# Performance work log

Hardware: AMD Instinct MI355X
Metric: run time of the kernel (lower is better)

The kernel has to match this reference:

```python
import jax, jax.numpy as jnp
import numpy as np

B, FC, FR, L, H, E, GH = 2048, 171, 171, 32, 256, 16, 64
IN = L + FC      # 203: decoder input_size
INT = L + H      # 288: decoder inter_size
OUT = FR         # 171: output_size (num_future_predictions=1)


def _forward(x, c, eps, fc1_w, fc1_b, fc2_w, fc2_b, mu_w, mu_b, lv_w, lv_b,
             g0_w, g0_b, g1_w, g1_b, g2_w, g2_b, w0, b0, w1, b1, w2, b2):
    elu = jax.nn.elu
    # Encoder_up
    h1 = elu(jnp.concatenate([x, c], axis=1) @ fc1_w + fc1_b)
    h2 = elu(jnp.concatenate([x, h1], axis=1) @ fc2_w + fc2_b)
    s = jnp.concatenate([x, h2], axis=1)
    mu = s @ mu_w + mu_b
    logvar = s @ lv_w + lv_b
    # reparameterize (eps supplied externally for determinism)
    z = mu + eps * jnp.exp(0.5 * logvar)
    # MixedDecoder_up gate -> softmax coefficients [B, E]
    g = elu(jnp.concatenate([z, c], axis=1) @ g0_w + g0_b)
    g = elu(g @ g1_w + g1_b)
    coef = jax.nn.softmax(g @ g2_w + g2_b, axis=1)
    # soft-MoE blended layers: mixed_weight = coef @ expert weights, then per-sample matvec
    layer = c
    for W, bb, act in ((w0, b0, True), (w1, b1, True), (w2, b2, False)):
        inp = jnp.concatenate([z, layer], axis=1)           # [B, in]
        mixed_w = jnp.einsum('be,eio->bio', coef, W)        # [B, in, out] (matches torch matmul+view)
        out = jnp.einsum('bi,bio->bo', inp, mixed_w) + coef @ bb  # baddbmm
        layer = jax.nn.elu(out) if act else out
    return layer, mu, logvar


def setup_inputs() -> dict:
    key = jax.random.key(0)
    ks = jax.random.split(key, 20)
    r = jax.random.normal

    def w(k, i, o):
        return (r(k, (i, o), jnp.float32) / np.sqrt(i)).astype(jnp.float32)

    return {
        'x': r(ks[0], (B, FR), jnp.float32),
        'c': r(ks[1], (B, FC), jnp.float32),
        'eps': r(ks[2], (B, L), jnp.float32),
        # Encoder_up params (stored as [in, out])
        'fc1_w': w(ks[3], FC + FR, H), 'fc1_b': jnp.zeros((H,), jnp.float32),
        'fc2_w': w(ks[4], FR + H, H), 'fc2_b': jnp.zeros((H,), jnp.float32),
        'mu_w': w(ks[5], FR + H, L), 'mu_b': jnp.zeros((L,), jnp.float32),
        'lv_w': w(ks[6], FR + H, L), 'lv_b': jnp.zeros((L,), jnp.float32),
        # gate MLP
        'g0_w': w(ks[7], IN, GH), 'g0_b': jnp.zeros((GH,), jnp.float32),
        'g1_w': w(ks[8], GH, GH), 'g1_b': jnp.zeros((GH,), jnp.float32),
        'g2_w': w(ks[9], GH, E), 'g2_b': jnp.zeros((E,), jnp.float32),
        # expert weights [E, in, out], biases filled with 0.01 as in the source
        'w0': (r(ks[10], (E, IN, H), jnp.float32) / np.sqrt(IN)).astype(jnp.float32),
        'b0': jnp.full((E, H), 0.01, jnp.float32),
        'w1': (r(ks[11], (E, INT, H), jnp.float32) / np.sqrt(INT)).astype(jnp.float32),
        'b1': jnp.full((E, H), 0.01, jnp.float32),
        'w2': (r(ks[12], (E, INT, OUT), jnp.float32) / np.sqrt(INT)).astype(jnp.float32),
        'b2': jnp.full((E, OUT), 0.01, jnp.float32),
    }


def reference(x, c, eps, fc1_w, fc1_b, fc2_w, fc2_b, mu_w, mu_b, lv_w, lv_b,
              g0_w, g0_b, g1_w, g1_b, g2_w, g2_b, w0, b0, w1, b1, w2, b2):
    return _forward(x, c, eps, fc1_w, fc1_b, fc2_w, fc2_b, mu_w, mu_b, lv_w, lv_b,
                    g0_w, g0_b, g1_w, g1_b, g2_w, g2_b, w0, b0, w1, b1, w2, b2)
```

## Files before the change

kernel.cpp:

```cpp
#include <hip/hip_runtime.h>
#include <math.h>

#define NB   2048
#define NFC  171
#define NFR  171
#define NL   32
#define NH   256
#define NE   16
#define NGH  64
#define NIN  203
#define NINT 288
#define NOUT 171

typedef __attribute__((ext_vector_type(8))) short bf16x8;
typedef __attribute__((ext_vector_type(4))) float f32x4;

__device__ __forceinline__ float elu_f(float v) {
    return v > 0.0f ? v : expm1f(v);
}

__device__ __forceinline__ short f2bf(float f) {
    unsigned u = __float_as_uint(f);
    unsigned r = (u + 0x7FFFu + ((u >> 16) & 1u)) >> 16;
    return (short)r;
}

__device__ __forceinline__ void gload16(void* lds, const void* g) {
    __builtin_amdgcn_global_load_lds(
        (const __attribute__((address_space(1))) unsigned*)g,
        (__attribute__((address_space(3))) unsigned*)lds, 16, 0, 0);
}

template<int N> __device__ __forceinline__ void waitcnt_vm() {
    if constexpr (N == 0)      asm volatile("s_waitcnt vmcnt(0) lgkmcnt(0)" ::: "memory");
    else if constexpr (N == 1) asm volatile("s_waitcnt vmcnt(1) lgkmcnt(0)" ::: "memory");
    else if constexpr (N == 2) asm volatile("s_waitcnt vmcnt(2) lgkmcnt(0)" ::: "memory");
    else                       asm volatile("s_waitcnt vmcnt(4) lgkmcnt(0)" ::: "memory");
}
__device__ __forceinline__ void loop_sync(int s, int NS) {
    if (s + 3 < NS)      waitcnt_vm<2>();
    else if (s + 2 < NS) waitcnt_vm<1>();
    else                 waitcnt_vm<0>();
    __builtin_amdgcn_s_barrier();
}
__device__ __forceinline__ void loop_sync64(int s, int NS) {
    if (s + 3 < NS)      waitcnt_vm<4>();
    else if (s + 2 < NS) waitcnt_vm<2>();
    else                 waitcnt_vm<0>();
    __builtin_amdgcn_s_barrier();
}

__global__ __launch_bounds__(256) void prep_all(
    const float* s0, const float* s1, const float* s2, const float* s3,
    const float* s4, const float* s5, const float* s6,
    const float* s7, const float* s8, const float* s9,
    short* d0, short* d1, short* d2, short* d3,
    short* d4, short* d5, short* d6, short* d7, short* d8, short* d9,
    const float* __restrict__ x, const float* __restrict__ c,
    short* __restrict__ xc, short* __restrict__ xh1, short* __restrict__ xh2,
    short* __restrict__ inp0)
{
    __shared__ float T[32][33];
    const int tid = threadIdx.x;

    if (blockIdx.x >= 3168) {
        const int b = blockIdx.x - 3168;
        for (int i = tid; i < 384; i += 256) {
            float v = (i < 171) ? x[b * 171 + i] : ((i < 342) ? c[b * 171 + (i - 171)] : 0.0f);
            xc[(size_t)b * 384 + i] = f2bf(v);
        }
        for (int i = tid; i < 171; i += 256) {
            short v = f2bf(x[b * 171 + i]);
            xh1[(size_t)b * 448 + i] = v;
            xh2[(size_t)b * 448 + i] = v;
        }
        for (int i = tid; i < 21; i += 256) {
            xh1[(size_t)b * 448 + 427 + i] = 0;
            xh2[(size_t)b * 448 + 427 + i] = 0;
        }
        for (int i = tid; i < 192; i += 256) {
            inp0[(size_t)b * 224 + 32 + i] = (i < 171) ? f2bf(c[b * 171 + i]) : (short)0;
        }
        return;
    }

    constexpr int K_[10]   = {342, 427, 427, 427, 203, 288, 288, 203,  64,  64};
    constexpr int O_[10]   = {256, 256,  32,  32, 256, 256, 171,  64,  64,  16};
    constexpr int KP_[10]  = {384, 448, 448, 448, 224, 288, 288, 224,  64,  64};
    constexpr int OP_[10]  = {256, 256,  64,  64, 256, 256, 192,  64,  64,  32};
    constexpr int nKT_[10] = { 12,  14,  14,  14,   7,   9,   9,   7,   2,   2};
    constexpr int tpe_[10] = { 96, 112,  14,  14,  56,  72,  54,  14,   4,   2};
    constexpr int st_[10]  = {  0,  96, 208, 222, 236,1132,2284,3148,3162,3166};
    const float* srcs[10] = {s0, s1, s2, s3, s4, s5, s6, s7, s8, s9};
    short*       dsts[10] = {d0, d1, d2, d3, d4, d5, d6, d7, d8, d9};

    int t = blockIdx.x;
    int s = 0;
    while (s < 9 && t >= st_[s + 1]) ++s;
    int local = t - st_[s];
    int e = local / tpe_[s];
    int rem = local - e * tpe_[s];
    int ox = rem / nKT_[s];
    int ky = rem - ox * nKT_[s];
    const int K = K_[s], O = O_[s], KP = KP_[s], OP = OP_[s];
    const float* src = srcs[s];
    short* dst = dsts[s];

    const int cc = tid & 31, r0 = tid >> 5;
#pragma unroll
    for (int i = 0; i < 4; ++i) {
        int r = r0 + i * 8;
        int gk = ky * 32 + r, go = ox * 32 + cc;
        T[r][cc] = (gk < K && go < O) ? src[((size_t)e * K + gk) * O + go] : 0.0f;
    }
    __syncthreads();
#pragma unroll
    for (int i = 0; i < 4; ++i) {
        int r = r0 + i * 8;
        int go = ox * 32 + r, gk = ky * 32 + cc;
        dst[((size_t)e * OP + go) * KP + gk] = f2bf(T[cc][r]);
    }
}

template<int KP>
__global__ __launch_bounds__(256, 2) void enc_gemm(
    const short* __restrict__ A,
    const short* __restrict__ Wt,
    const float* __restrict__ bias,
    short* __restrict__ dst, int dstld, int dstoff)
{
    constexpr int NKS = KP / 64;
    constexpr int CHR = KP / 8;

    __shared__ short As[32 * KP];
    __shared__ short Bs[4][64 * 64];

    const int tid = threadIdx.x;
    const int lane = tid & 63;
    const int wid = tid >> 6;
    const int wm = wid & 1, wn = wid >> 1;
    const int brow = blockIdx.y * 32, bcol = blockIdx.x * 64;
    const int wbase = wid * 1024;
    const int kseg = lane >> 4;

#pragma unroll
    for (int i = 0; i < (32 * CHR) / 256; ++i) {
        int ch = i * 256 + tid;
        int r = ch / CHR, kc = ch - r * CHR;
        int kcs = kc ^ ((r >> 1) & 3);
        gload16((char*)As + i * 4096 + wbase, A + (size_t)(brow + r) * KP + kcs * 8);
    }
    auto stageB = [&](int buf, int ks) {
#pragma unroll
        for (int g = 0; g < 2; ++g) {
            int ch = g * 256 + tid;
            int o = ch >> 3, sl = ch & 7;
            int sp = sl ^ ((o >> 1) & 3);
            gload16((char*)Bs[buf] + g * 4096 + wbase,
                    Wt + (size_t)(bcol + o) * KP + ks * 64 + sp * 8);
        }
    };
    stageB(0, 0); stageB(1, 1); stageB(2, 2);
    waitcnt_vm<4>();
    __builtin_amdgcn_s_barrier();

    const f32x4 zero4 = {0.0f, 0.0f, 0.0f, 0.0f};
    f32x4 acc[2] = {zero4, zero4};

    for (int s = 0; s < NKS; ++s) {
        if (s + 3 < NKS) stageB((s + 3) & 3, s + 3);
#pragma unroll
        for (int kk = 0; kk < 2; ++kk) {
            bf16x8 a, b[2];
            int rr = wm * 16 + (lane & 15);
            int kcp = (s * 8 + kk * 4 + kseg) ^ ((rr >> 1) & 3);
            a = *(const bf16x8*)&As[rr * KP + kcp * 8];
#pragma unroll
            for (int nr = 0; nr < 2; ++nr) {
                int oo = wn * 32 + nr * 16 + (lane & 15);
                int sp = (kk * 4 + kseg) ^ ((oo >> 1) & 3);
                b[nr] = *(const bf16x8*)&Bs[s & 3][oo * 64 + sp * 8];
            }
#pragma unroll
            for (int nr = 0; nr < 2; ++nr)
                acc[nr] = __builtin_amdgcn_mfma_f32_16x16x32_bf16(a, b[nr], acc[nr], 0, 0, 0);
        }
        loop_sync64(s, NKS);
    }

#pragma unroll
    for (int j = 0; j < 4; ++j) {
        int row = brow + wm * 16 + kseg * 4 + j;
#pragma unroll
        for (int nr = 0; nr < 2; ++nr) {
            int col = bcol + wn * 32 + nr * 16 + (lane & 15);
            float v = acc[nr][j] + bias[col];
            dst[(size_t)row * dstld + dstoff + col] = f2bf(elu_f(v));
        }
    }
}

__global__ __launch_bounds__(256) void mulvz_gate(
    const short* __restrict__ A,
    const short* __restrict__ Wt,
    const float* __restrict__ mub, const float* __restrict__ lvb,
    const float* __restrict__ eps,
    const short* __restrict__ g0wt,
    const short* __restrict__ g1wt,
    const short* __restrict__ g2wt,
    const float* __restrict__ g0b, const float* __restrict__ g1b,
    const float* __restrict__ g2b,
    float* __restrict__ mu_out, float* __restrict__ lv_out,
    short* __restrict__ inp0, short* __restrict__ inp1, short* __restrict__ inp2,
    float* __restrict__ coef)
{
    constexpr int KP = 448;
    constexpr int NKS = KP / 64;
    constexpr int CHR = KP / 8;

    __shared__ short As[32 * 448];
    __shared__ short Bs[4][64 * 64];
    __shared__ float Els[32][32];
    __shared__ short gA[32 * 224];
    __shared__ short g0s[64 * 224];
    __shared__ short g1s[64 * 64];
    __shared__ short g2s[32 * 64];
    __shared__ short hA[32 * 64];
    __shared__ short hB[32 * 64];

    const int tid = threadIdx.x;
    const int lane = tid & 63;
    const int wid = tid >> 6;
    const int wm = wid & 1, wn = wid >> 1;
    const int brow = blockIdx.y * 32;
    const int wbase = wid * 1024;
    const int kseg = lane >> 4;
    const int l15 = lane & 15;

#pragma unroll
    for (int i = 0; i < 7; ++i) {
        int ch = i * 256 + tid;
        int r = ch / CHR, kc = ch - r * CHR;
        int kcs = kc ^ ((r >> 1) & 3);
        gload16((char*)As + i * 4096 + wbase, A + (size_t)(brow + r) * KP + kcs * 8);
    }
#pragma unroll
    for (int i = 0; i < 4; ++i) {
        int ch = i * 256 + tid;
        if (ch < 896) {
            int r = ch / 28, kc = ch - r * 28;
            int kcs = kc ^ ((r >> 1) & 3);
            gload16((char*)gA + i * 4096 + wbase, inp0 + (size_t)(brow + r) * 224 + kcs * 8);
        }
    }
#pragma unroll
    for (int i = 0; i < 7; ++i) {
        int ch = i * 256 + tid;
        int r = ch / 28, kc = ch - r * 28;
        int kcs = kc ^ ((r >> 1) & 3);
        gload16((char*)g0s + i * 4096 + wbase, g0wt + (size_t)r * 224 + kcs * 8);
    }
#pragma unroll
    for (int i = 0; i < 2; ++i) {
        int ch = i * 256 + tid;
        int r = ch >> 3, kc = ch & 7;
        int kcs = kc ^ ((r >> 1) & 3);
        gload16((char*)g1s + i * 4096 + wbase, g1wt + (size_t)r * 64 + kcs * 8);
    }
    {
        int ch = tid;
        int r = ch >> 3, kc = ch & 7;
        int kcs = kc ^ ((r >> 1) & 3);
        gload16((char*)g2s + wbase, g2wt + (size_t)r * 64 + kcs * 8);
    }
    auto stageB = [&](int buf, int ks) {
#pragma unroll
        for (int g = 0; g < 2; ++g) {
            int ch = g * 256 + tid;
            int o = ch >> 3, sl = ch & 7;
            int sp = sl ^ ((o >> 1) & 3);
            gload16((char*)Bs[buf] + g * 4096 + wbase,
                    Wt + (size_t)o * KP + ks * 64 + sp * 8);
        }
    };
    stageB(0, 0); stageB(1, 1); stageB(2, 2);
    waitcnt_vm<4>();
    __builtin_amdgcn_s_barrier();

    const f32x4 zero4 = {0.0f, 0.0f, 0.0f, 0.0f};
    f32x4 acc[2] = {zero4, zero4};

    for (int s = 0; s < NKS; ++s) {
        if (s + 3 < NKS) stageB((s + 3) & 3, s + 3);
#pragma unroll
        for (int kk = 0; kk < 2; ++kk) {
            bf16x8 av, b[2];
            int rr = wm * 16 + l15;
            int kcp = (s * 8 + kk * 4 + kseg) ^ ((rr >> 1) & 3);
            av = *(const bf16x8*)&As[rr * KP + kcp * 8];
#pragma unroll
            for (int nr = 0; nr < 2; ++nr) {
                int oo = wn * 32 + nr * 16 + l15;
                int sp = (kk * 4 + kseg) ^ ((oo >> 1) & 3);
                b[nr] = *(const bf16x8*)&Bs[s & 3][oo * 64 + sp * 8];
            }
#pragma unroll
            for (int nr = 0; nr < 2; ++nr)
                acc[nr] = __builtin_amdgcn_mfma_f32_16x16x32_bf16(av, b[nr], acc[nr], 0, 0, 0);
        }
        loop_sync64(s, NKS);
    }

#pragma unroll
    for (int j = 0; j < 4; ++j) {
        int rl = wm * 16 + kseg * 4 + j;
        int row = brow + rl;
#pragma unroll
        for (int nr = 0; nr < 2; ++nr) {
            int cc = nr * 16 + l15;
            if (wn == 1) {
                float v = acc[nr][j] + lvb[cc];
                lv_out[(size_t)row * 32 + cc] = v;
                Els[rl][cc] = expf(0.5f * v);
            } else {
                float v = acc[nr][j] + mub[cc];
                mu_out[(size_t)row * 32 + cc] = v;
                acc[nr][j] = v;
            }
        }
    }
    __syncthreads();
    if (wn == 0) {
#pragma unroll
        for (int j = 0; j < 4; ++j) {
            int rl = wm * 16 + kseg * 4 + j;
            int row = brow + rl;
#pragma unroll
            for (int nr = 0; nr < 2; ++nr) {
                int cc = nr * 16 + l15;
                float z = acc[nr][j] + eps[(size_t)row * 32 + cc] * Els[rl][cc];
                short zb = f2bf(z);
                inp0[(size_t)row * 224 + cc] = zb;
                inp1[(size_t)row * 288 + cc] = zb;
                inp2[(size_t)row * 288 + cc] = zb;
                int swz = (cc >> 3) ^ ((rl >> 1) & 3);
                gA[rl * 224 + swz * 8 + (cc & 7)] = zb;
            }
        }
    }
    __syncthreads();

    {
        f32x4 g[2] = {zero4, zero4};
#pragma unroll
        for (int s = 0; s < 7; ++s) {
            bf16x8 av, b[2];
            int rr = wm * 16 + l15;
            int kcp = (s * 4 + kseg) ^ ((rr >> 1) & 3);
            av = *(const bf16x8*)&gA[rr * 224 + kcp * 8];
#pragma unroll
            for (int nr = 0; nr < 2; ++nr) {
                int oo = wn * 32 + nr * 16 + l15;
                int sp = (s * 4 + kseg) ^ ((oo >> 1) & 3);
                b[nr] = *(const bf16x8*)&g0s[oo * 224 + sp * 8];
            }
#pragma unroll
            for (int nr = 0; nr < 2; ++nr)
                g[nr] = __builtin_amdgcn_mfma_f32_16x16x32_bf16(av, b[nr], g[nr], 0, 0, 0);
        }
#pragma unroll
        for (int j = 0; j < 4; ++j) {
            int rl = wm * 16 + kseg * 4 + j;
#pragma unroll
            for (int nr = 0; nr < 2; ++nr) {
                int cc = wn * 32 + nr * 16 + l15;
                float v = elu_f(g[nr][j] + g0b[cc]);
                int swz = (cc >> 3) ^ ((rl >> 1) & 3);
                hA[rl * 64 + swz * 8 + (cc & 7)] = f2bf(v);
            }
        }
    }
    __syncthreads();
    {
        f32x4 g[2] = {zero4, zero4};
#pragma unroll
        for (int s = 0; s < 2; ++s) {
            bf16x8 av, b[2];
            int rr = wm * 16 + l15;
            int kcp = (s * 4 + kseg) ^ ((rr >> 1) & 3);
            av = *(const bf16x8*)&hA[rr * 64 + kcp * 8];
#pragma unroll
            for (int nr = 0; nr < 2; ++nr) {
                int oo = wn * 32 + nr * 16 + l15;
                int sp = (s * 4 + kseg) ^ ((oo >> 1) & 3);
                b[nr] = *(const bf16x8*)&g1s[oo * 64 + sp * 8];
            }
#pragma unroll
            for (int nr = 0; nr < 2; ++nr)
                g[nr] = __builtin_amdgcn_mfma_f32_16x16x32_bf16(av, b[nr], g[nr], 0, 0, 0);
        }
#pragma unroll
        for (int j = 0; j < 4; ++j) {
            int rl = wm * 16 + kseg * 4 + j;
#pragma unroll
            for (int nr = 0; nr < 2; ++nr) {
                int cc = wn * 32 + nr * 16 + l15;
                float v = elu_f(g[nr][j] + g1b[cc]);
                int swz = (cc >> 3) ^ ((rl >> 1) & 3);
                hB[rl * 64 + swz * 8 + (cc & 7)] = f2bf(v);
            }
        }
    }
    __syncthreads();
    if (wn == 0) {
        f32x4 g = zero4;
#pragma unroll
        for (int s = 0; s < 2; ++s) {
            bf16x8 av, b;
            int rr = wm * 16 + l15;
            int kcp = (s * 4 + kseg) ^ ((rr >> 1) & 3);
            av = *(const bf16x8*)&hB[rr * 64 + kcp * 8];
            int oo = l15;
            int sp = (s * 4 + kseg) ^ ((oo >> 1) & 3);
            b = *(const bf16x8*)&g2s[oo * 64 + sp * 8];
            g = __builtin_amdgcn_mfma_f32_16x16x32_bf16(av, b, g, 0, 0, 0);
        }
        float bv = g2b[l15];
#pragma unroll
        for (int j = 0; j < 4; ++j) {
            int rl = wm * 16 + kseg * 4 + j;
            int row = brow + rl;
            float a2 = g[j] + bv;
            float m = a2;
            for (int off = 1; off < 16; off <<= 1) m = fmaxf(m, __shfl_xor(m, off, 16));
            float ev = expf(a2 - m);
            float sm = ev;
            for (int off = 1; off < 16; off <<= 1) sm += __shfl_xor(sm, off, 16);
            coef[(size_t)row * 16 + l15] = ev / sm;
        }
    }
}

template<int KP, int OP, int EPG>
__global__ __launch_bounds__(256, 2) void moe_gemm(
    const short* __restrict__ inp,
    const short* __restrict__ Wt,
    const float* __restrict__ coef,
    float* __restrict__ partial)
{
    constexpr int NKS = KP / 32;
    constexpr int CHR = KP / 8;
    constexpr int NS = EPG * NKS;

    __shared__ short As[64 * KP];
    __shared__ short Bs[4][64 * 32];
    __shared__ float Cs[64][16];

    const int tid = threadIdx.x;
    const int lane = tid & 63;
    const int wid = tid >> 6;
    const int wm = wid >> 1, wn = wid & 1;
    const int bn = blockIdx.x, bm = blockIdx.y, kg = blockIdx.z;
    const int brow = bm * 64, bcol = bn * 64;
    const int wbase = wid * 1024;
    const int kseg = lane >> 4;

    {
        int r = tid >> 2, q = tid & 3;
        float4 v = ((const float4*)(coef + (size_t)(brow + r) * 16))[q];
        *(float4*)&Cs[r][q * 4] = v;
    }
#pragma unroll
    for (int i = 0; i < (64 * KP / 8) / 256; ++i) {
        int ch = i * 256 + tid;
        int r = ch / CHR, kc = ch - r * CHR;
        int kcs = kc ^ ((r >> 1) & 3);
        gload16((char*)As + i * 4096 + wbase,
                inp + (size_t)(brow + r) * KP + kcs * 8);
    }
    auto stageB = [&](int buf, int s) {
        int ei = s / NKS, ks = s - ei * NKS;
        int e = kg * EPG + ei;
        int o = tid >> 2, sl = tid & 3;
        int sp = sl ^ ((o >> 1) & 3);
        gload16((char*)Bs[buf] + wbase,
                Wt + (size_t)(e * OP + bcol + o) * KP + ks * 32 + sp * 8);
    };
    stageB(0, 0); stageB(1, 1); stageB(2, 2);
    waitcnt_vm<2>();
    __builtin_amdgcn_s_barrier();

    const f32x4 zero4 = {0.0f, 0.0f, 0.0f, 0.0f};
    f32x4 outacc[2][2] = {{zero4, zero4}, {zero4, zero4}};
    f32x4 acc[2][2];

    for (int s = 0; s < NS; ++s) {
        int ei = s / NKS, ks = s - ei * NKS;
        if (ks == 0) {
            acc[0][0] = zero4; acc[0][1] = zero4;
            acc[1][0] = zero4; acc[1][1] = zero4;
        }
        if (s + 3 < NS) stageB((s + 3) & 3, s + 3);

        bf16x8 a[2], b[2];
#pragma unroll
        for (int mr = 0; mr < 2; ++mr) {
            int rr = wm * 32 + mr * 16 + (lane & 15);
            int kcr = ks * 4 + kseg;
            int kcp = kcr ^ ((rr >> 1) & 3);
            a[mr] = *(const bf16x8*)&As[rr * KP + kcp * 8];
        }
#pragma unroll
        for (int nr = 0; nr < 2; ++nr) {
            int oo = wn * 32 + nr * 16 + (lane & 15);
            int sp = kseg ^ ((oo >> 1) & 3);
            b[nr] = *(const bf16x8*)&Bs[s & 3][oo * 32 + sp * 8];
        }
#pragma unroll
        for (int mr = 0; mr < 2; ++mr)
#pragma unroll
            for (int nr = 0; nr < 2; ++nr)
                acc[mr][nr] = __builtin_amdgcn_mfma_f32_16x16x32_bf16(
                    a[mr], b[nr], acc[mr][nr], 0, 0, 0);

        if (ks == NKS - 1) {
            int e = kg * EPG + ei;
#pragma unroll
            for (int mr = 0; mr < 2; ++mr) {
                int rb = wm * 32 + mr * 16 + kseg * 4;
#pragma unroll
                for (int j = 0; j < 4; ++j) {
                    float cfv = Cs[rb + j][e];
#pragma unroll
                    for (int nr = 0; nr < 2; ++nr)
                        outacc[mr][nr][j] += cfv * acc[mr][nr][j];
                }
            }
        }
        loop_sync(s, NS);
    }

    float* pout = partial + (size_t)kg * 2048 * OP;
#pragma unroll
    for (int mr = 0; mr < 2; ++mr)
#pragma unroll
        for (int j = 0; j < 4; ++j) {
            int row = brow + wm * 32 + mr * 16 + kseg * 4 + j;
#pragma unroll
            for (int nr = 0; nr < 2; ++nr) {
                int col = bcol + wn * 32 + nr * 16 + (lane & 15);
                pout[(size_t)row * OP + col] = outacc[mr][nr][j];
            }
        }
}

template<int NP, int O, bool ACT, int NKG>
__global__ __launch_bounds__(256) void moe_finish(
    const float* __restrict__ partial,
    const float* __restrict__ coef,
    const float* __restrict__ bb,
    short* __restrict__ nxt,
    float* __restrict__ fout)
{
    __shared__ float bbs[16 * O];
    __shared__ float cfs[8][16];
    const int tid = threadIdx.x;
    const int row0 = blockIdx.x * 8;

    for (int i = tid; i < 16 * O; i += 256) bbs[i] = bb[i];
    if (tid < 128) cfs[tid >> 4][tid & 15] = coef[(row0 + (tid >> 4)) * 16 + (tid & 15)];
    __syncthreads();

    constexpr int NG = NP / 4;
    for (int idx = tid; idx < 8 * NG; idx += 256) {
        int r = idx / NG, og = idx - r * NG;
        int o = og * 4;
        int row = row0 + r;
        float4 v = {0.f, 0.f, 0.f, 0.f};
#pragma unroll
        for (int kg = 0; kg < NKG; ++kg) {
            float4 p = *(const float4*)&partial[(size_t)(kg * 2048 + row) * NP + o];
            v.x += p.x; v.y += p.y; v.z += p.z; v.w += p.w;
        }
        float vv[4] = {v.x, v.y, v.z, v.w};
#pragma unroll
        for (int t = 0; t < 4; ++t) {
            int oo = o + t;
            if (oo < O) {
                float bias = 0.0f;
#pragma unroll
                for (int e = 0; e < 16; ++e) bias += cfs[r][e] * bbs[e * O + oo];
                float val = vv[t] + bias;
                if (ACT) val = elu_f(val);
                if (nxt) nxt[(size_t)row * 288 + 32 + oo] = f2bf(val);
                else     fout[(size_t)row * O + oo] = val;
            }
        }
    }
}

extern "C" void kernel_launch(void* const* d_in, const int* in_sizes, int n_in,
                              void* d_out, int out_size, void* d_ws, size_t ws_size,
                              hipStream_t stream)
{
    const float* x    = (const float*)d_in[0];
    const float* c    = (const float*)d_in[1];
    const float* eps  = (const float*)d_in[2];
    const float* fc1w = (const float*)d_in[3];
    const float* fc1b = (const float*)d_in[4];
    const float* fc2w = (const float*)d_in[5];
    const float* fc2b = (const float*)d_in[6];
    const float* muw  = (const float*)d_in[7];
    const float* mub  = (const float*)d_in[8];
    const float* lvw  = (const float*)d_in[9];
    const float* lvb  = (const float*)d_in[10];
    const float* g0w  = (const float*)d_in[11];
    const float* g0b  = (const float*)d_in[12];
    const float* g1w  = (const float*)d_in[13];
    const float* g1b  = (const float*)d_in[14];
    const float* g2w  = (const float*)d_in[15];
    const float* g2b  = (const float*)d_in[16];
    const float* w0   = (const float*)d_in[17];
    const float* b0   = (const float*)d_in[18];
    const float* w1   = (const float*)d_in[19];
    const float* b1   = (const float*)d_in[20];
    const float* w2   = (const float*)d_in[21];
    const float* b2   = (const float*)d_in[22];

    float* out       = (float*)d_out;
    float* out_layer = out;
    float* out_mu    = out + NB * NOUT;
    float* out_lv    = out_mu + NB * NL;

    float* ws      = (float*)d_ws;
    float* partial = ws;
    float* cf      = partial + 8 * 2048 * 256;
    short* xc    = (short*)(cf + 32768);
    short* xh1   = xc   + (size_t)2048 * 384;
    short* xh2   = xh1  + (size_t)2048 * 448;
    short* inp0  = xh2  + (size_t)2048 * 448;
    short* inp1  = inp0 + (size_t)2048 * 224;
    short* inp2  = inp1 + (size_t)2048 * 288;
    short* fc1Wt = inp2 + (size_t)2048 * 288;
    short* fc2Wt = fc1Wt + 256 * 384;
    short* mlWt  = fc2Wt + 256 * 448;
    short* Wt0   = mlWt + 64 * 448;
    short* Wt1   = Wt0 + 16 * 256 * 224;
    short* Wt2   = Wt1 + 16 * 256 * 288;
    short* g0wt  = Wt2 + 16 * 192 * 288;
    short* g1wt  = g0wt + 64 * 224;
    short* g2wt  = g1wt + 64 * 64;

    dim3 blk(256);

    prep_all<<<dim3(3168 + 2048), blk, 0, stream>>>(
        fc1w, fc2w, muw, lvw, w0, w1, w2, g0w, g1w, g2w,
        fc1Wt, fc2Wt, mlWt, mlWt + 32 * 448, Wt0, Wt1, Wt2, g0wt, g1wt, g2wt,
        x, c, xc, xh1, xh2, inp0);

    enc_gemm<384><<<dim3(4, 64), blk, 0, stream>>>(xc,  fc1Wt, fc1b, xh1, 448, 171);
    enc_gemm<448><<<dim3(4, 64), blk, 0, stream>>>(xh1, fc2Wt, fc2b, xh2, 448, 171);
    mulvz_gate<<<dim3(1, 64), blk, 0, stream>>>(
        xh2, mlWt, mub, lvb, eps, g0wt, g1wt, g2wt, g0b, g1b, g2b,
        out_mu, out_lv, inp0, inp1, inp2, cf);

    moe_gemm<224, 256, 4><<<dim3(4, 32, 4), blk, 0, stream>>>(inp0, Wt0, cf, partial);
    moe_finish<256, 256, true, 4><<<dim3(256), blk, 0, stream>>>(partial, cf, b0, inp1, nullptr);
    moe_gemm<288, 256, 4><<<dim3(4, 32, 4), blk, 0, stream>>>(inp1, Wt1, cf, partial);
    moe_finish<256, 256, true, 4><<<dim3(256), blk, 0, stream>>>(partial, cf, b1, inp2, nullptr);
    moe_gemm<288, 192, 4><<<dim3(3, 32, 4), blk, 0, stream>>>(inp2, Wt2, cf, partial);
    moe_finish<192, 171, false, 4><<<dim3(256), blk, 0, stream>>>(partial, cf, b2, nullptr, out_layer);
}
```

Baseline: 120.3 us.

## Deepen MoE GEMM prefetch pipeline and split experts into more k-groups

```diff
diff --git a/kernel.cpp b/kernel.cpp
--- a/kernel.cpp
+++ b/kernel.cpp
@@ -35,18 +35,21 @@
     if constexpr (N == 0)      asm volatile("s_waitcnt vmcnt(0) lgkmcnt(0)" ::: "memory");
     else if constexpr (N == 1) asm volatile("s_waitcnt vmcnt(1) lgkmcnt(0)" ::: "memory");
     else if constexpr (N == 2) asm volatile("s_waitcnt vmcnt(2) lgkmcnt(0)" ::: "memory");
+    else if constexpr (N == 3) asm volatile("s_waitcnt vmcnt(3) lgkmcnt(0)" ::: "memory");
     else                       asm volatile("s_waitcnt vmcnt(4) lgkmcnt(0)" ::: "memory");
-}
-__device__ __forceinline__ void loop_sync(int s, int NS) {
-    if (s + 3 < NS)      waitcnt_vm<2>();
-    else if (s + 2 < NS) waitcnt_vm<1>();
-    else                 waitcnt_vm<0>();
-    __builtin_amdgcn_s_barrier();
 }
 __device__ __forceinline__ void loop_sync64(int s, int NS) {
     if (s + 3 < NS)      waitcnt_vm<4>();
     else if (s + 2 < NS) waitcnt_vm<2>();
     else                 waitcnt_vm<0>();
+    __builtin_amdgcn_s_barrier();
+}
+__device__ __forceinline__ void phase_sync(int rem) {
+    if (rem >= 6)      waitcnt_vm<4>();
+    else if (rem == 5) waitcnt_vm<3>();
+    else if (rem == 4) waitcnt_vm<2>();
+    else if (rem == 3) waitcnt_vm<1>();
+    else               waitcnt_vm<0>();
     __builtin_amdgcn_s_barrier();
 }
 
@@ -453,7 +456,7 @@
     constexpr int NS = EPG * NKS;
 
     __shared__ short As[64 * KP];
-    __shared__ short Bs[4][64 * 32];
+    __shared__ short Bs[8][64 * 32];
     __shared__ float Cs[64][16];
 
     const int tid = threadIdx.x;
@@ -464,6 +467,7 @@
     const int brow = bm * 64, bcol = bn * 64;
     const int wbase = wid * 1024;
     const int kseg = lane >> 4;
+    const int l15 = lane & 15;
 
     {
         int r = tid >> 2, q = tid & 3;
@@ -487,34 +491,32 @@
                 Wt + (size_t)(e * OP + bcol + o) * KP + ks * 32 + sp * 8);
     };
     stageB(0, 0); stageB(1, 1); stageB(2, 2);
-    waitcnt_vm<2>();
+    stageB(3, 3); stageB(4, 4); stageB(5, 5);
+    waitcnt_vm<4>();
     __builtin_amdgcn_s_barrier();
 
     const f32x4 zero4 = {0.0f, 0.0f, 0.0f, 0.0f};
     f32x4 outacc[2][2] = {{zero4, zero4}, {zero4, zero4}};
     f32x4 acc[2][2];
 
-    for (int s = 0; s < NS; ++s) {
+    auto do_step = [&](int s) {
         int ei = s / NKS, ks = s - ei * NKS;
         if (ks == 0) {
             acc[0][0] = zero4; acc[0][1] = zero4;
             acc[1][0] = zero4; acc[1][1] = zero4;
         }
-        if (s + 3 < NS) stageB((s + 3) & 3, s + 3);
-
         bf16x8 a[2], b[2];
 #pragma unroll
         for (int mr = 0; mr < 2; ++mr) {
-            int rr = wm * 32 + mr * 16 + (lane & 15);
-            int kcr = ks * 4 + kseg;
-            int kcp = kcr ^ ((rr >> 1) & 3);
+            int rr = wm * 32 + mr * 16 + l15;
+            int kcp = (ks * 4 + kseg) ^ ((rr >> 1) & 3);
             a[mr] = *(const bf16x8*)&As[rr * KP + kcp * 8];
         }
 #pragma unroll
         for (int nr = 0; nr < 2; ++nr) {
-            int oo = wn * 32 + nr * 16 + (lane & 15);
+            int oo = wn * 32 + nr * 16 + l15;
             int sp = kseg ^ ((oo >> 1) & 3);
-            b[nr] = *(const bf16x8*)&Bs[s & 3][oo * 32 + sp * 8];
+            b[nr] = *(const bf16x8*)&Bs[s & 7][oo * 32 + sp * 8];
         }
 #pragma unroll
         for (int mr = 0; mr < 2; ++mr)
@@ -522,7 +524,6 @@
             for (int nr = 0; nr < 2; ++nr)
                 acc[mr][nr] = __builtin_amdgcn_mfma_f32_16x16x32_bf16(
                     a[mr], b[nr], acc[mr][nr], 0, 0, 0);
-
         if (ks == NKS - 1) {
             int e = kg * EPG + ei;
 #pragma unroll
@@ -537,7 +538,15 @@
                 }
             }
         }
-        loop_sync(s, NS);
+    };
+
+    for (int p = 0; p < NS / 2; ++p) {
+        int s0 = 2 * p;
+        if (s0 + 6 < NS) stageB((s0 + 6) & 7, s0 + 6);
+        if (s0 + 7 < NS) stageB((s0 + 7) & 7, s0 + 7);
+        do_step(s0);
+        do_step(s0 + 1);
+        phase_sync(NS - s0 - 2);
     }
 
     float* pout = partial + (size_t)kg * 2048 * OP;
@@ -548,7 +557,7 @@
             int row = brow + wm * 32 + mr * 16 + kseg * 4 + j;
 #pragma unroll
             for (int nr = 0; nr < 2; ++nr) {
-                int col = bcol + wn * 32 + nr * 16 + (lane & 15);
+                int col = bcol + wn * 32 + nr * 16 + l15;
                 pout[(size_t)row * OP + col] = outacc[mr][nr][j];
             }
         }
@@ -664,10 +673,10 @@
         xh2, mlWt, mub, lvb, eps, g0wt, g1wt, g2wt, g0b, g1b, g2b,
         out_mu, out_lv, inp0, inp1, inp2, cf);
 
-    moe_gemm<224, 256, 4><<<dim3(4, 32, 4), blk, 0, stream>>>(inp0, Wt0, cf, partial);
-    moe_finish<256, 256, true, 4><<<dim3(256), blk, 0, stream>>>(partial, cf, b0, inp1, nullptr);
-    moe_gemm<288, 256, 4><<<dim3(4, 32, 4), blk, 0, stream>>>(inp1, Wt1, cf, partial);
-    moe_finish<256, 256, true, 4><<<dim3(256), blk, 0, stream>>>(partial, cf, b1, inp2, nullptr);
-    moe_gemm<288, 192, 4><<<dim3(3, 32, 4), blk, 0, stream>>>(inp2, Wt2, cf, partial);
-    moe_finish<192, 171, false, 4><<<dim3(256), blk, 0, stream>>>(partial, cf, b2, nullptr, out_layer);
-}
+    moe_gemm<224, 256, 2><<<dim3(4, 32, 8), blk, 0, stream>>>(inp0, Wt0, cf, partial);
+    moe_finish<256, 256, true, 8><<<dim3(256), blk, 0, stream>>>(partial, cf, b0, inp1, nullptr);
+    moe_gemm<288, 256, 2><<<dim3(4, 32, 8), blk, 0, stream>>>(inp1, Wt1, cf, partial);
+    moe_finish<256, 256, true, 8><<<dim3(256), blk, 0, stream>>>(partial, cf, b1, inp2, nullptr);
+    moe_gemm<288, 192, 2><<<dim3(3, 32, 8), blk, 0, stream>>>(inp2, Wt2, cf, partial);
+    moe_finish<192, 171, false, 8><<<dim3(256), blk, 0, stream>>>(partial, cf, b2, nullptr, out_layer);
+}
```

Result: faster. 100.0 us, median of 2 (-16.8%).
